# Kernel optimization log

Hardware: AMD Instinct MI355X
Metric: run time of the kernel (lower is better)

Reference implementation:

```python
import jax, jax.numpy as jnp
import numpy as np
import math

L, B, T, C, H, DH, V, MEM = 6, 2, 1024, 1024, 16, 64, 32000, 128

def _ln(x, g, b):
    m = jnp.mean(x, -1, keepdims=True)
    v = jnp.mean((x - m) ** 2, -1, keepdims=True)
    return (x - m) * jax.lax.rsqrt(v + 1e-5) * g + b

def _rel_shift(x):
    # x: [B,H,Q,K]; TransformerXL shift trick: pad zero col, reshape, drop first row
    b, h, q, k = x.shape
    xp = jnp.pad(x, ((0, 0), (0, 0), (0, 0), (1, 0)))
    xp = xp.reshape(b, h, k + 1, q)
    return xp[:, :, 1:, :].reshape(b, h, q, k)

def setup_inputs():
    key = jax.random.key(0)
    ks = jax.random.split(key, 12)
    d = {}
    d['idx'] = jax.random.randint(ks[0], (B, T), 0, V)
    d['mems'] = jax.random.normal(ks[1], (L, B, MEM, C), dtype=jnp.float32) * 0.02
    d['wte'] = jax.random.normal(ks[2], (V, C), dtype=jnp.float32) * 0.02
    d['ln1_g'] = jnp.ones((L, C), jnp.float32); d['ln1_b'] = jnp.zeros((L, C), jnp.float32)
    d['attn_w'] = jax.random.normal(ks[3], (L, C, 3 * C), dtype=jnp.float32) * 0.02
    d['attn_b'] = jnp.zeros((L, 3 * C), jnp.float32)
    d['proj_w'] = jax.random.normal(ks[4], (L, C, C), dtype=jnp.float32) * 0.02
    d['proj_b'] = jnp.zeros((L, C), jnp.float32)
    d['r_emb'] = jax.random.normal(ks[5], (L, H, DH), dtype=jnp.float32) * 0.02
    d['r_bias'] = jax.random.normal(ks[6], (L, H, DH), dtype=jnp.float32) * 0.02
    d['ln2_g'] = jnp.ones((L, C), jnp.float32); d['ln2_b'] = jnp.zeros((L, C), jnp.float32)
    d['fc_w'] = jax.random.normal(ks[7], (L, C, 4 * C), dtype=jnp.float32) * 0.02
    d['fc_b'] = jnp.zeros((L, 4 * C), jnp.float32)
    d['fc2_w'] = jax.random.normal(ks[8], (L, 4 * C, C), dtype=jnp.float32) * 0.02
    d['fc2_b'] = jnp.zeros((L, C), jnp.float32)
    d['lnf_g'] = jnp.ones((C,), jnp.float32); d['lnf_b'] = jnp.zeros((C,), jnp.float32)
    d['lm_w'] = jax.random.normal(ks[9], (C, V), dtype=jnp.float32) * 0.02
    return d

def _attn(x, mem, w, b, pw, pb, remb, rbias):
    Bx, Tx, Cx = x.shape
    cat = jnp.concatenate([mem, x], axis=1)          # [B,K,C], K = mem_len + Tx
    K = cat.shape[1]
    qkv = cat @ w + b
    q, k, v = jnp.split(qkv, 3, axis=-1)
    q = q.reshape(Bx, K, H, DH).transpose(0, 2, 1, 3)
    k = k.reshape(Bx, K, H, DH).transpose(0, 2, 1, 3)
    v = v.reshape(Bx, K, H, DH).transpose(0, 2, 1, 3)
    q = q + rbias[None, :, None, :]
    AC = jnp.einsum('bhid,bhjd->bhij', q, k)
    # BD: r is r_emb broadcast over positions, so q@r^T is constant over j
    s = jnp.einsum('bhid,hd->bhi', q, remb)
    BD = _rel_shift(jnp.broadcast_to(s[..., None], (Bx, H, K, K)))
    p = jax.nn.softmax((AC + BD) / math.sqrt(DH), axis=-1)
    y = jnp.einsum('bhij,bhjd->bhid', p, v).transpose(0, 2, 1, 3).reshape(Bx, K, Cx)
    y = y @ pw + pb
    new_mem = cat[:, -MEM:]
    return y, new_mem

def reference(idx, mems, wte, ln1_g, ln1_b, attn_w, attn_b, proj_w, proj_b, r_emb, r_bias, ln2_g, ln2_b, fc_w, fc_b, fc2_w, fc2_b, lnf_g, lnf_b, lm_w):
    x = wte[idx]                                      # [B,T,C]
    new_mems = []
    for l in range(L):
        h = _ln(x, ln1_g[l], ln1_b[l])
        y, nm = _attn(h, mems[l], attn_w[l], attn_b[l], proj_w[l], proj_b[l], r_emb[l], r_bias[l])
        h2 = _ln(y, ln2_g[l], ln2_b[l])
        m = jax.nn.gelu(h2 @ fc_w[l] + fc_b[l], approximate=False) @ fc2_w[l] + fc2_b[l]
        x = y + m                                     # note: residual onto attn output (length grows by MEM per layer)
        new_mems.append(nm)
    x = _ln(x, lnf_g, lnf_b)
    logits = x @ lm_w                                 # [B, L*MEM+T, V]
    return logits, jnp.stack(new_mems)
```

## Files before the change

kernel.cpp:

```cpp
#include <hip/hip_runtime.h>
#include <hip/hip_bf16.h>
#include <hip/hip_fp16.h>

#define LNUM 6
#define BB 2
#define TT 1024
#define CC 1024
#define HH 16
#define DHH 64
#define VV 32000
#define MM 128

typedef _Float16 f16;
typedef _Float16 f16x8 __attribute__((ext_vector_type(8)));
typedef float f32x4 __attribute__((ext_vector_type(4)));

__device__ __forceinline__ void g2lds16(const void* g, void* l) {
    __builtin_amdgcn_global_load_lds((const __attribute__((address_space(1))) void*)g,
                                     (__attribute__((address_space(3))) void*)l,
                                     16, 0, 0);
}

__device__ __forceinline__ float wred(float v) {
#pragma unroll
    for (int o = 32; o > 0; o >>= 1) v += __shfl_xor(v, o);
    return v;
}

__global__ __launch_bounds__(256)
void transpose_k(const float* __restrict__ W, f16* __restrict__ WT, int R, int Cc)
{
    __shared__ float tile[32][33];
    const size_t base = (size_t)blockIdx.z * R * Cc;
    const int c0 = blockIdx.x * 32, r0 = blockIdx.y * 32;
    const int tx = threadIdx.x & 31, ty = threadIdx.x >> 5;
#pragma unroll
    for (int i = 0; i < 32; i += 8)
        tile[ty + i][tx] = W[base + (size_t)(r0 + ty + i) * Cc + c0 + tx];
    __syncthreads();
#pragma unroll
    for (int i = 0; i < 32; i += 8)
        WT[base + (size_t)(c0 + ty + i) * R + r0 + tx] = (f16)tile[tx][ty + i];
}

__global__ __launch_bounds__(256)
void embed_k(const int* __restrict__ idx, const float* __restrict__ wte, float* __restrict__ X)
{
    const int row = blockIdx.x;
    const int id = idx[row];
    const float4* src = (const float4*)(wte + (size_t)id * CC);
    float4* dst = (float4*)(X + (size_t)row * CC);
    dst[threadIdx.x] = src[threadIdx.x];
}

__global__ __launch_bounds__(256)
void ln_k(const float* __restrict__ X, const float* __restrict__ g,
          const float* __restrict__ bta, f16* __restrict__ outH)
{
    const int row = blockIdx.x * 4 + (threadIdx.x >> 6);
    const int lane = threadIdx.x & 63;
    const float4* xr = (const float4*)(X + (size_t)row * CC);
    float4 v[4];
    float s = 0.f;
#pragma unroll
    for (int i = 0; i < 4; ++i) { v[i] = xr[i * 64 + lane]; s += v[i].x + v[i].y + v[i].z + v[i].w; }
    s = wred(s);
    const float mean = s * (1.f / CC);
    float q = 0.f;
#pragma unroll
    for (int i = 0; i < 4; ++i) {
        float a = v[i].x - mean, b = v[i].y - mean, c = v[i].z - mean, d = v[i].w - mean;
        q += a * a + b * b + c * c + d * d;
    }
    q = wred(q);
    const float rs = rsqrtf(q * (1.f / CC) + 1e-5f);
    const float4* g4 = (const float4*)g;
    const float4* b4 = (const float4*)bta;
    uint2* orow = (uint2*)(outH + (size_t)row * CC);
#pragma unroll
    for (int i = 0; i < 4; ++i) {
        float4 gg = g4[i * 64 + lane], bb = b4[i * 64 + lane];
        union { f16 h4[4]; uint2 u; } pk;
        pk.h4[0] = (f16)((v[i].x - mean) * rs * gg.x + bb.x);
        pk.h4[1] = (f16)((v[i].y - mean) * rs * gg.y + bb.y);
        pk.h4[2] = (f16)((v[i].z - mean) * rs * gg.z + bb.z);
        pk.h4[3] = (f16)((v[i].w - mean) * rs * gg.w + bb.w);
        orow[i * 64 + lane] = pk.u;
    }
}

__global__ __launch_bounds__(256)
void ln1cat_k(const float* __restrict__ X, const float* __restrict__ memsL,
              const float* __restrict__ g, const float* __restrict__ bta,
              f16* __restrict__ catH, float* __restrict__ nmOut,
              int K, int Kin)
{
    const int row = blockIdx.x * 4 + (threadIdx.x >> 6);
    const int lane = threadIdx.x & 63;
    const int b = row / K, rr = row % K;
    uint2* crow = (uint2*)(catH + (size_t)row * CC);
    if (rr < MM) {
        const float4* src = (const float4*)(memsL + ((size_t)b * MM + rr) * CC);
#pragma unroll
        for (int i = 0; i < 4; ++i) {
            float4 vv = src[i * 64 + lane];
            union { f16 h4[4]; uint2 u; } pk;
            pk.h4[0] = (f16)vv.x; pk.h4[1] = (f16)vv.y; pk.h4[2] = (f16)vv.z; pk.h4[3] = (f16)vv.w;
            crow[i * 64 + lane] = pk.u;
        }
        return;
    }
    const float4* xr = (const float4*)(X + ((size_t)b * Kin + (rr - MM)) * CC);
    float4 v[4];
    float s = 0.f;
#pragma unroll
    for (int i = 0; i < 4; ++i) { v[i] = xr[i * 64 + lane]; s += v[i].x + v[i].y + v[i].z + v[i].w; }
    s = wred(s);
    const float mean = s * (1.f / CC);
    float q = 0.f;
#pragma unroll
    for (int i = 0; i < 4; ++i) {
        float a = v[i].x - mean, b2 = v[i].y - mean, c = v[i].z - mean, d = v[i].w - mean;
        q += a * a + b2 * b2 + c * c + d * d;
    }
    q = wred(q);
    const float rs = rsqrtf(q * (1.f / CC) + 1e-5f);
    const float4* g4 = (const float4*)g;
    const float4* b4 = (const float4*)bta;
    float4* nm = nullptr;
    if (rr >= K - MM) nm = (float4*)(nmOut + ((size_t)b * MM + (rr - (K - MM))) * CC);
#pragma unroll
    for (int i = 0; i < 4; ++i) {
        float4 gg = g4[i * 64 + lane], bb = b4[i * 64 + lane];
        float4 o;
        o.x = (v[i].x - mean) * rs * gg.x + bb.x;
        o.y = (v[i].y - mean) * rs * gg.y + bb.y;
        o.z = (v[i].z - mean) * rs * gg.z + bb.z;
        o.w = (v[i].w - mean) * rs * gg.w + bb.w;
        union { f16 h4[4]; uint2 u; } pk;
        pk.h4[0] = (f16)o.x; pk.h4[1] = (f16)o.y; pk.h4[2] = (f16)o.z; pk.h4[3] = (f16)o.w;
        crow[i * 64 + lane] = pk.u;
        if (nm) nm[i * 64 + lane] = o;
    }
}

template <int EPI>
__global__ __launch_bounds__(256, 2)
void gemm_k(const f16* __restrict__ A, const f16* __restrict__ BT,
            const float* __restrict__ bias, const float* __restrict__ res,
            float* __restrict__ outF, f16* __restrict__ outH,
            int M, int N, int Kc)
{
    __shared__ f16 sA[128 * 32];
    __shared__ f16 sB[128 * 32];
    const int bn = blockIdx.x, bm = blockIdx.y;
    const int tid = threadIdx.x;
    const int w = tid >> 6, l = tid & 63;
    const int wr = w >> 1, wc = w & 1;
    const int lr = l & 15, lk = (l >> 4) * 8;

    f32x4 acc[4][4] = {};

    const int ar = w * 32 + (l >> 2);
    const int ak = (l & 3) * 8;
    const f16* gA = A + (size_t)(bm * 128 + ar) * Kc + ak;
    const f16* gB = BT + (size_t)(bn * 128 + ar) * Kc + ak;
    f16* lA = sA + w * 1024;
    f16* lB = sB + w * 1024;

    for (int kt = 0; kt < Kc; kt += 32) {
        g2lds16(gA + kt, lA);
        g2lds16(gA + kt + (size_t)16 * Kc, lA + 512);
        g2lds16(gB + kt, lB);
        g2lds16(gB + kt + (size_t)16 * Kc, lB + 512);
        __syncthreads();
        f16x8 af[4], bf[4];
#pragma unroll
        for (int mi = 0; mi < 4; ++mi) af[mi] = *(const f16x8*)&sA[(wr * 64 + mi * 16 + lr) * 32 + lk];
#pragma unroll
        for (int ni = 0; ni < 4; ++ni) bf[ni] = *(const f16x8*)&sB[(wc * 64 + ni * 16 + lr) * 32 + lk];
#pragma unroll
        for (int mi = 0; mi < 4; ++mi)
#pragma unroll
            for (int ni = 0; ni < 4; ++ni)
                acc[mi][ni] = __builtin_amdgcn_mfma_f32_16x16x32_f16(af[mi], bf[ni], acc[mi][ni], 0, 0, 0);
        __syncthreads();
    }

    const int orow0 = bm * 128 + wr * 64 + (l >> 4) * 4;
    const int ocol0 = bn * 128 + wc * 64 + lr;
#pragma unroll
    for (int mi = 0; mi < 4; ++mi)
#pragma unroll
        for (int ni = 0; ni < 4; ++ni) {
            const int col = ocol0 + ni * 16;
            const float bv = (EPI >= 1) ? bias[col] : 0.f;
#pragma unroll
            for (int r = 0; r < 4; ++r) {
                const int row = orow0 + mi * 16 + r;
                float v = acc[mi][ni][r] + bv;
                if (EPI == 2) {
                    v = 0.5f * v * (1.f + erff(v * 0.70710678118654752f));
                    outH[(size_t)row * N + col] = (f16)v;
                } else if (EPI == 4) {
                    outH[(size_t)row * N + col] = (f16)v;
                } else if (EPI == 3) {
                    v += res[(size_t)row * N + col];
                    outF[(size_t)row * N + col] = v;
                } else {
                    outF[(size_t)row * N + col] = v;
                }
            }
        }
}

template <int EPI>
__global__ __launch_bounds__(512, 2)
void gemm256_k(const f16* __restrict__ A, const f16* __restrict__ BT,
               const float* __restrict__ bias,
               float* __restrict__ outF, f16* __restrict__ outH,
               int M, int N, int Kc)
{
    __shared__ char ldsbuf[131072];
    char* ldsA = ldsbuf;
    char* ldsB = ldsbuf + 65536;

    const int nbn = N >> 8;
    const int nwg = gridDim.x;
    {
    }
    int id = blockIdx.x;
    const int qq = nwg >> 3, rr8 = nwg & 7;
    const int xcd = id & 7, pos = id >> 3;
    const int wgid = (xcd < rr8 ? xcd * (qq + 1) : rr8 * (qq + 1) + (xcd - rr8) * qq) + pos;
    const int bm = wgid / nbn, bn = wgid % nbn;

    const int t_ = threadIdx.x;
    const int w = t_ >> 6, l = t_ & 63;
    const int wm = w >> 2, wn = w & 3;
    const int lr = l & 15, lhi = l >> 4;

    const f16* gA = A + (size_t)bm * 256 * Kc;
    const f16* gB = BT + (size_t)bn * 256 * Kc;

    auto stage = [&](const f16* Gbase, char* ldsHalf, int kt) {
#pragma unroll
        for (int ii = 0; ii < 2; ++ii) {
            const int gb = (w << 1) + ii;
            const int s = (gb << 6) + l;
            const int row = s >> 3, grp = s & 7;
            g2lds16(Gbase + (size_t)row * Kc + kt + ((grp ^ (row & 7)) << 3),
                    ldsHalf + gb * 1024);
        }
    };
    auto rdfrag = [&](const char* halfBase, int rowInHalf, int ks) -> f16x8 {
        return *(const f16x8*)(halfBase + rowInHalf * 128 +
                               ((((ks << 2) + lhi) ^ (rowInHalf & 7)) << 4));
    };

    f32x4 acc[8][4] = {};
    f16x8 aA[4][2], blo[2][2], bhi[2][2];

    const int NT = Kc >> 6;
    const char* aHalf0 = ldsA + wm * 16384;
    const char* aHalf1 = ldsA + 32768 + wm * 16384;
    const char* bHalf0 = ldsB + (wn >> 1) * 16384;
    const char* bHalf1 = ldsB + 32768 + (wn >> 1) * 16384;
    const int brow = (wn & 1) * 64;

    stage(gA, ldsA + 0, 0);
    stage(gA + (size_t)128 * Kc, ldsA + 16384, 0);
    stage(gB, ldsB + 0, 0);
    stage(gB + (size_t)128 * Kc, ldsB + 16384, 0);
    stage(gB, ldsB + 32768, 64);
    stage(gB + (size_t)128 * Kc, ldsB + 49152, 64);
    asm volatile("s_waitcnt vmcnt(0)" ::: "memory");
    __builtin_amdgcn_s_barrier();

#define MFMA_QUAD(MQ, NQ, BR)                                                            \
    __builtin_amdgcn_s_setprio(1);                                                       \
    _Pragma("unroll") for (int mf = 0; mf < 4; ++mf)                                     \
    _Pragma("unroll") for (int nf = 0; nf < 2; ++nf)                                     \
    _Pragma("unroll") for (int ks = 0; ks < 2; ++ks)                                     \
        acc[(MQ)*4 + mf][(NQ)*2 + nf] =                                                  \
            __builtin_amdgcn_mfma_f32_16x16x32_f16(aA[mf][ks], BR[nf][ks],               \
                                                   acc[(MQ)*4 + mf][(NQ)*2 + nf], 0, 0, 0); \
    __builtin_amdgcn_s_setprio(0);

#define PHASE_SYNC()                                          \
    __builtin_amdgcn_s_barrier();                             \
    asm volatile("s_waitcnt lgkmcnt(0)" ::: "memory");        \
    __builtin_amdgcn_sched_barrier(0);

    for (int t = 0; t < NT; t += 2) {
        const bool pf0 = (t + 2) < NT;
        const int kb = (t + 1) << 6, kc2 = (t + 2) << 6, kd = (t + 3) << 6;

#pragma unroll
        for (int mf = 0; mf < 4; ++mf)
#pragma unroll
            for (int ks = 0; ks < 2; ++ks) aA[mf][ks] = rdfrag(aHalf0, mf * 16 + lr, ks);
#pragma unroll
        for (int nf = 0; nf < 2; ++nf)
#pragma unroll
            for (int ks = 0; ks < 2; ++ks) blo[nf][ks] = rdfrag(bHalf0, brow + nf * 16 + lr, ks);
        stage(gA, ldsA + 32768, kb);
        PHASE_SYNC();
        MFMA_QUAD(0, 0, blo);
        __builtin_amdgcn_s_barrier();

#pragma unroll
        for (int nf = 0; nf < 2; ++nf)
#pragma unroll
            for (int ks = 0; ks < 2; ++ks) bhi[nf][ks] = rdfrag(bHalf0, brow + 32 + nf * 16 + lr, ks);
        stage(gA + (size_t)128 * Kc, ldsA + 49152, kb);
        PHASE_SYNC();
        MFMA_QUAD(0, 1, bhi);
        __builtin_amdgcn_s_barrier();

#pragma unroll
        for (int mf = 0; mf < 4; ++mf)
#pragma unroll
            for (int ks = 0; ks < 2; ++ks) aA[mf][ks] = rdfrag(aHalf0, 64 + mf * 16 + lr, ks);
        if (pf0) stage(gB, ldsB + 0, kc2);
        PHASE_SYNC();
        MFMA_QUAD(1, 0, blo);
        __builtin_amdgcn_s_barrier();

        if (pf0) {
            stage(gB + (size_t)128 * Kc, ldsB + 16384, kc2);
            asm volatile("s_waitcnt vmcnt(4)" ::: "memory");
        } else {
            asm volatile("s_waitcnt vmcnt(0)" ::: "memory");
        }
        PHASE_SYNC();
        MFMA_QUAD(1, 1, bhi);
        __builtin_amdgcn_s_barrier();

#pragma unroll
        for (int mf = 0; mf < 4; ++mf)
#pragma unroll
            for (int ks = 0; ks < 2; ++ks) aA[mf][ks] = rdfrag(aHalf1, mf * 16 + lr, ks);
#pragma unroll
        for (int nf = 0; nf < 2; ++nf)
#pragma unroll
            for (int ks = 0; ks < 2; ++ks) blo[nf][ks] = rdfrag(bHalf1, brow + nf * 16 + lr, ks);
        if (pf0) stage(gA, ldsA + 0, kc2);
        PHASE_SYNC();
        MFMA_QUAD(0, 0, blo);
        __builtin_amdgcn_s_barrier();

#pragma unroll
        for (int nf = 0; nf < 2; ++nf)
#pragma unroll
            for (int ks = 0; ks < 2; ++ks) bhi[nf][ks] = rdfrag(bHalf1, brow + 32 + nf * 16 + lr, ks);
        if (pf0) stage(gA + (size_t)128 * Kc, ldsA + 16384, kc2);
        PHASE_SYNC();
        MFMA_QUAD(0, 1, bhi);
        __builtin_amdgcn_s_barrier();

#pragma unroll
        for (int mf = 0; mf < 4; ++mf)
#pragma unroll
            for (int ks = 0; ks < 2; ++ks) aA[mf][ks] = rdfrag(aHalf1, 64 + mf * 16 + lr, ks);
        if (pf0) stage(gB, ldsB + 32768, kd);
        PHASE_SYNC();
        MFMA_QUAD(1, 0, blo);
        __builtin_amdgcn_s_barrier();

        if (pf0) {
            stage(gB + (size_t)128 * Kc, ldsB + 49152, kd);
            asm volatile("s_waitcnt vmcnt(4)" ::: "memory");
        } else {
            asm volatile("s_waitcnt vmcnt(0)" ::: "memory");
        }
        PHASE_SYNC();
        MFMA_QUAD(1, 1, bhi);
        __builtin_amdgcn_s_barrier();
    }
#undef MFMA_QUAD
#undef PHASE_SYNC

    const int rb0 = bm * 256 + wm * 128 + lhi * 4;
    const int cb0 = bn * 256 + wn * 64 + lr;
#pragma unroll
    for (int mf = 0; mf < 8; ++mf)
#pragma unroll
        for (int nf = 0; nf < 4; ++nf) {
            const int col = cb0 + nf * 16;
            const float bv = (EPI >= 1) ? bias[col] : 0.f;
#pragma unroll
            for (int r = 0; r < 4; ++r) {
                const int row = rb0 + mf * 16 + r;
                float v = acc[mf][nf][r] + bv;
                if (EPI == 2) {
                    v = 0.5f * v * (1.f + erff(v * 0.70710678118654752f));
                    outH[(size_t)row * N + col] = (f16)v;
                } else if (EPI == 4) {
                    outH[(size_t)row * N + col] = (f16)v;
                } else {
                    outF[(size_t)row * N + col] = v;
                }
            }
        }
}

__global__ __launch_bounds__(256)
void attn_k(const f16* __restrict__ qkv, const float* __restrict__ remb,
            const float* __restrict__ rbias, f16* __restrict__ yH, int K)
{
    __shared__ f16 K_lds[64 * 64];
    __shared__ f16 Vt_lds[64 * 64];
    __shared__ f16 P_lds[64 * 64];
    __shared__ float s_s[66];

    const int b = blockIdx.x >> 4, h = blockIdx.x & 15;
    const int i0 = blockIdx.y * 64;
    const int t = threadIdx.x;
    const int w = t >> 6, l = t & 63;
    const int c = l & 15, g = l >> 4;

    const f16* qg = qkv + (size_t)b * K * 3072 + h * 64;
    const f16* kg = qg + 1024;
    const f16* vg = qg + 2048;
    const float* rb = rbias + h * 64;
    const float* re = remb + h * 64;

    f16x8 qf[2];
    {
        const int qrow = i0 + w * 16 + c;
#pragma unroll
        for (int ks = 0; ks < 2; ++ks) {
            f16x8 raw = *(const f16x8*)(qg + (size_t)qrow * 3072 + ks * 32 + g * 8);
            f16x8 o;
#pragma unroll
            for (int j = 0; j < 8; ++j) o[j] = (f16)((float)raw[j] + rb[ks * 32 + g * 8 + j]);
            qf[ks] = o;
        }
    }
    if (t < 65) {
        float sv = 0.f;
        const int i = i0 + t;
        if (i < K) {
            const f16* qr = qg + (size_t)i * 3072;
#pragma unroll
            for (int d8 = 0; d8 < 8; ++d8) {
                f16x8 v8 = *(const f16x8*)(qr + d8 * 8);
#pragma unroll
                for (int j = 0; j < 8; ++j) sv += ((float)v8[j] + rb[d8 * 8 + j]) * re[d8 * 8 + j];
            }
        }
        s_s[t] = sv;
    }
    __syncthreads();

    float sA[4], sB[4];
#pragma unroll
    for (int r = 0; r < 4; ++r) {
        sA[r] = s_s[w * 16 + g * 4 + r];
        sB[r] = s_s[w * 16 + g * 4 + r + 1];
    }

    float m_run[4] = {-1e30f, -1e30f, -1e30f, -1e30f};
    float l_run[4] = {0.f, 0.f, 0.f, 0.f};
    f32x4 yacc[4] = {};

    const int kb = t >> 4, db = t & 15;

    for (int j0 = 0; j0 < K; j0 += 64) {
#pragma unroll
        for (int i = 0; i < 2; ++i) {
            const int slot = w * 128 + i * 64 + l;
            const int row = slot >> 3, grp = slot & 7;
            const f16* src = kg + (size_t)(j0 + row) * 3072 + ((grp ^ (row & 7)) * 8);
            g2lds16(src, (char*)K_lds + (size_t)(w * 128 + i * 64) * 16);
        }
        {
            union { uint2 u; f16 hh[4]; } rowv[4];
#pragma unroll
            for (int i = 0; i < 4; ++i)
                rowv[i].u = *(const uint2*)(vg + (size_t)(j0 + kb * 4 + i) * 3072 + db * 4);
#pragma unroll
            for (int j = 0; j < 4; ++j) {
                union { uint2 u; f16 hh[4]; } colv;
#pragma unroll
                for (int i = 0; i < 4; ++i) colv.hh[i] = rowv[i].hh[j];
                const int d = db * 4 + j;
                *(uint2*)((char*)Vt_lds + d * 128 + ((kb * 8) ^ ((d & 7) << 4))) = colv.u;
            }
        }
        __syncthreads();

        f32x4 sc[4] = {};
#pragma unroll
        for (int tt = 0; tt < 4; ++tt) {
            const int row = tt * 16 + c;
#pragma unroll
            for (int ks = 0; ks < 2; ++ks) {
                f16x8 kf = *(const f16x8*)((char*)K_lds + row * 128 + ((ks * 64 + g * 16) ^ ((row & 7) << 4)));
                sc[tt] = __builtin_amdgcn_mfma_f32_16x16x32_f16(qf[ks], kf, sc[tt], 0, 0, 0);
            }
        }

        float p[4][4];
#pragma unroll
        for (int tt = 0; tt < 4; ++tt)
#pragma unroll
            for (int r = 0; r < 4; ++r) {
                const int gi = i0 + w * 16 + g * 4 + r;
                const int gj = j0 + tt * 16 + c;
                const float bd = (gj <= gi) ? sA[r] : ((gj == gi + 1) ? 0.f : sB[r]);
                p[tt][r] = (sc[tt][r] + bd) * 0.125f;
            }
#pragma unroll
        for (int r = 0; r < 4; ++r) {
            float mx = fmaxf(fmaxf(p[0][r], p[1][r]), fmaxf(p[2][r], p[3][r]));
            mx = fmaxf(mx, __shfl_xor(mx, 1));
            mx = fmaxf(mx, __shfl_xor(mx, 2));
            mx = fmaxf(mx, __shfl_xor(mx, 4));
            mx = fmaxf(mx, __shfl_xor(mx, 8));
            const float mnew = fmaxf(m_run[r], mx);
            const float f = __expf(m_run[r] - mnew);
            m_run[r] = mnew;
            float ss = 0.f;
#pragma unroll
            for (int tt = 0; tt < 4; ++tt) {
                const float e = __expf(p[tt][r] - mnew);
                p[tt][r] = e;
                ss += e;
            }
            ss += __shfl_xor(ss, 1);
            ss += __shfl_xor(ss, 2);
            ss += __shfl_xor(ss, 4);
            ss += __shfl_xor(ss, 8);
            l_run[r] = l_run[r] * f + ss;
#pragma unroll
            for (int tt = 0; tt < 4; ++tt) yacc[tt][r] *= f;
        }

#pragma unroll
        for (int tt = 0; tt < 4; ++tt)
#pragma unroll
            for (int r = 0; r < 4; ++r) {
                const int q = w * 16 + g * 4 + r;
                *(f16*)((char*)P_lds + q * 128 + (((tt * 16 + c) * 2) ^ ((q & 7) << 4))) = (f16)p[tt][r];
            }
        asm volatile("s_waitcnt lgkmcnt(0)" ::: "memory");
        __builtin_amdgcn_sched_barrier(0);

        {
            const int qrow = w * 16 + c;
            f16x8 pa[2];
#pragma unroll
            for (int ks = 0; ks < 2; ++ks)
                pa[ks] = *(const f16x8*)((char*)P_lds + qrow * 128 + ((ks * 64 + g * 16) ^ ((qrow & 7) << 4)));
#pragma unroll
            for (int tt = 0; tt < 4; ++tt) {
                const int drow = tt * 16 + c;
#pragma unroll
                for (int ks = 0; ks < 2; ++ks) {
                    f16x8 vb = *(const f16x8*)((char*)Vt_lds + drow * 128 + ((ks * 64 + g * 16) ^ ((drow & 7) << 4)));
                    yacc[tt] = __builtin_amdgcn_mfma_f32_16x16x32_f16(pa[ks], vb, yacc[tt], 0, 0, 0);
                }
            }
        }
        __syncthreads();
    }

#pragma unroll
    for (int r = 0; r < 4; ++r) {
        const float inv = 1.f / l_run[r];
        const int row = i0 + w * 16 + g * 4 + r;
        f16* dst = yH + (size_t)(b * K + row) * CC + h * 64;
#pragma unroll
        for (int tt = 0; tt < 4; ++tt)
            dst[tt * 16 + c] = (f16)(yacc[tt][r] * inv);
    }
}

extern "C" void kernel_launch(void* const* d_in, const int* in_sizes, int n_in,
                              void* d_out, int out_size, void* d_ws, size_t ws_size,
                              hipStream_t stream)
{
    (void)in_sizes; (void)n_in; (void)out_size; (void)ws_size;
    const int*   idx    = (const int*)  d_in[0];
    const float* mems   = (const float*)d_in[1];
    const float* wte    = (const float*)d_in[2];
    const float* ln1_g  = (const float*)d_in[3];
    const float* ln1_b  = (const float*)d_in[4];
    const float* attn_w = (const float*)d_in[5];
    const float* attn_b = (const float*)d_in[6];
    const float* proj_w = (const float*)d_in[7];
    const float* proj_b = (const float*)d_in[8];
    const float* r_emb  = (const float*)d_in[9];
    const float* r_bias = (const float*)d_in[10];
    const float* ln2_g  = (const float*)d_in[11];
    const float* ln2_b  = (const float*)d_in[12];
    const float* fc_w   = (const float*)d_in[13];
    const float* fc_b   = (const float*)d_in[14];
    const float* fc2_w  = (const float*)d_in[15];
    const float* fc2_b  = (const float*)d_in[16];
    const float* lnf_g  = (const float*)d_in[17];
    const float* lnf_b  = (const float*)d_in[18];
    const float* lm_w   = (const float*)d_in[19];
    float* out = (float*)d_out;

    char* wp = (char*)d_ws; size_t off = 0;
    auto carve = [&](size_t bytes) -> void* {
        void* p = wp + off; off += (bytes + 255) & ~(size_t)255; return p;
    };
    const int KMAX = TT + LNUM * MM;
    f16*  attn_wT = (f16*) carve((size_t)LNUM * 3 * CC * CC * 2);
    f16*  proj_wT = (f16*) carve((size_t)LNUM * CC * CC * 2);
    f16*  fc_wT   = (f16*) carve((size_t)LNUM * 4 * CC * CC * 2);
    f16*  fc2_wT  = (f16*) carve((size_t)LNUM * 4 * CC * CC * 2);
    f16*  lm_wT   = (f16*) carve((size_t)VV * CC * 2);
    float* x0     = (float*)carve((size_t)BB * KMAX * CC * 4);
    float* x1     = (float*)carve((size_t)BB * KMAX * CC * 4);
    f16*  catH    = (f16*) carve((size_t)BB * KMAX * CC * 2);
    f16*  qkv16   = (f16*) carve((size_t)BB * KMAX * 3 * CC * 2);
    f16*  yH      = (f16*) carve((size_t)BB * KMAX * CC * 2);
    float* yp     = (float*)carve((size_t)BB * KMAX * CC * 4);
    f16*  h2H     = (f16*) carve((size_t)BB * KMAX * CC * 2);
    f16*  a1H     = (f16*) carve((size_t)BB * KMAX * 4 * CC * 2);
    f16*  xfH     = (f16*) carve((size_t)BB * KMAX * CC * 2);

    transpose_k<<<dim3(3 * CC / 32, CC / 32, LNUM), 256, 0, stream>>>(attn_w, attn_wT, CC, 3 * CC);
    transpose_k<<<dim3(CC / 32, CC / 32, LNUM),     256, 0, stream>>>(proj_w, proj_wT, CC, CC);
    transpose_k<<<dim3(4 * CC / 32, CC / 32, LNUM), 256, 0, stream>>>(fc_w, fc_wT, CC, 4 * CC);
    transpose_k<<<dim3(CC / 32, 4 * CC / 32, LNUM), 256, 0, stream>>>(fc2_w, fc2_wT, 4 * CC, CC);
    transpose_k<<<dim3(VV / 32, CC / 32, 1),        256, 0, stream>>>(lm_w, lm_wT, CC, VV);

    embed_k<<<BB * TT, 256, 0, stream>>>(idx, wte, x0);

    const size_t LOGITS = (size_t)BB * KMAX * VV;
    float* xcur = x0; float* xnxt = x1;
    for (int l = 0; l < LNUM; ++l) {
        const int Kin = TT + MM * l;
        const int K = Kin + MM;
        const int Mrows = BB * K;
        const int nbm = Mrows / 256;
        ln1cat_k<<<Mrows / 4, 256, 0, stream>>>(xcur, mems + (size_t)l * BB * MM * CC,
                                                ln1_g + l * CC, ln1_b + l * CC,
                                                catH, out + LOGITS + (size_t)l * BB * MM * CC, K, Kin);
        gemm256_k<4><<<nbm * (3 * CC / 256), 512, 0, stream>>>(
            catH, attn_wT + (size_t)l * 3 * CC * CC, attn_b + (size_t)l * 3 * CC,
            nullptr, qkv16, Mrows, 3 * CC, CC);
        attn_k<<<dim3(BB * HH, K / 64), 256, 0, stream>>>(
            qkv16, r_emb + (size_t)l * HH * DHH, r_bias + (size_t)l * HH * DHH, yH, K);
        gemm_k<1><<<dim3(CC / 128, Mrows / 128), 256, 0, stream>>>(
            yH, proj_wT + (size_t)l * CC * CC, proj_b + (size_t)l * CC, nullptr,
            yp, nullptr, Mrows, CC, CC);
        ln_k<<<Mrows / 4, 256, 0, stream>>>(yp, ln2_g + l * CC, ln2_b + l * CC, h2H);
        gemm256_k<2><<<nbm * (4 * CC / 256), 512, 0, stream>>>(
            h2H, fc_wT + (size_t)l * 4 * CC * CC, fc_b + (size_t)l * 4 * CC,
            nullptr, a1H, Mrows, 4 * CC, CC);
        gemm_k<3><<<dim3(CC / 128, Mrows / 128), 256, 0, stream>>>(
            a1H, fc2_wT + (size_t)l * 4 * CC * CC, fc2_b + (size_t)l * CC, yp,
            xnxt, nullptr, Mrows, CC, 4 * CC);
        float* tmp = xcur; xcur = xnxt; xnxt = tmp;
    }
    ln_k<<<(BB * KMAX) / 4, 256, 0, stream>>>(xcur, lnf_g, lnf_b, xfH);
    gemm256_k<0><<<(BB * KMAX / 256) * (VV / 256), 512, 0, stream>>>(
        xfH, lm_wT, nullptr, out, nullptr, BB * KMAX, VV, CC);
}
```

Baseline: 2.350 ms.

## Use lazy softmax rescaling, column-major 256 GEMM tiles, and 128-tile QKV/FC GEMMs

Flash attention now rescales the running max only when some lane's block max exceeds the current max by more than 8. It also defers the row-sum cross-lane reduction to the epilogue, which removes shuffles and exp/rescale work from the inner loop. The 256-tile GEMM now walks tiles with the M index fastest, so workgroups that share a weight column tile run close together. The QKV and FC1 projections move from the 256-tile kernel to the 128-tile gemm_k, trading per-block reuse for more blocks. The running max starts at 0 rather than -inf, so precision depends on scores staying bounded.

```diff
diff --git a/kernel.cpp b/kernel.cpp
--- a/kernel.cpp
+++ b/kernel.cpp
@@ -225,15 +225,13 @@
     char* ldsA = ldsbuf;
     char* ldsB = ldsbuf + 65536;
 
-    const int nbn = N >> 8;
+    const int nbm = M >> 8;
     const int nwg = gridDim.x;
-    {
-    }
     int id = blockIdx.x;
     const int qq = nwg >> 3, rr8 = nwg & 7;
     const int xcd = id & 7, pos = id >> 3;
     const int wgid = (xcd < rr8 ? xcd * (qq + 1) : rr8 * (qq + 1) + (xcd - rr8) * qq) + pos;
-    const int bm = wgid / nbn, bn = wgid % nbn;
+    const int bm = wgid % nbm, bn = wgid / nbm;
 
     const int t_ = threadIdx.x;
     const int w = t_ >> 6, l = t_ & 63;
@@ -461,8 +459,8 @@
         sB[r] = s_s[w * 16 + g * 4 + r + 1];
     }
 
-    float m_run[4] = {-1e30f, -1e30f, -1e30f, -1e30f};
-    float l_run[4] = {0.f, 0.f, 0.f, 0.f};
+    float m_run[4] = {0.f, 0.f, 0.f, 0.f};
+    float psum[4] = {0.f, 0.f, 0.f, 0.f};
     f32x4 yacc[4] = {};
 
     const int kb = t >> 4, db = t & 15;
@@ -512,30 +510,41 @@
                 const float bd = (gj <= gi) ? sA[r] : ((gj == gi + 1) ? 0.f : sB[r]);
                 p[tt][r] = (sc[tt][r] + bd) * 0.125f;
             }
+
+        float lmax[4];
+        bool need = false;
 #pragma unroll
         for (int r = 0; r < 4; ++r) {
-            float mx = fmaxf(fmaxf(p[0][r], p[1][r]), fmaxf(p[2][r], p[3][r]));
-            mx = fmaxf(mx, __shfl_xor(mx, 1));
-            mx = fmaxf(mx, __shfl_xor(mx, 2));
-            mx = fmaxf(mx, __shfl_xor(mx, 4));
-            mx = fmaxf(mx, __shfl_xor(mx, 8));
-            const float mnew = fmaxf(m_run[r], mx);
-            const float f = __expf(m_run[r] - mnew);
-            m_run[r] = mnew;
+            lmax[r] = fmaxf(fmaxf(p[0][r], p[1][r]), fmaxf(p[2][r], p[3][r]));
+            need |= (lmax[r] > m_run[r] + 8.f);
+        }
+        if (__any(need)) {
+#pragma unroll
+            for (int r = 0; r < 4; ++r) {
+                float mx = lmax[r];
+                mx = fmaxf(mx, __shfl_xor(mx, 1));
+                mx = fmaxf(mx, __shfl_xor(mx, 2));
+                mx = fmaxf(mx, __shfl_xor(mx, 4));
+                mx = fmaxf(mx, __shfl_xor(mx, 8));
+                if (mx > m_run[r]) {
+                    const float f = __expf(m_run[r] - mx);
+                    m_run[r] = mx;
+                    psum[r] *= f;
+#pragma unroll
+                    for (int tt = 0; tt < 4; ++tt) yacc[tt][r] *= f;
+                }
+            }
+        }
+#pragma unroll
+        for (int r = 0; r < 4; ++r) {
             float ss = 0.f;
 #pragma unroll
             for (int tt = 0; tt < 4; ++tt) {
-                const float e = __expf(p[tt][r] - mnew);
+                const float e = __expf(p[tt][r] - m_run[r]);
                 p[tt][r] = e;
                 ss += e;
             }
-            ss += __shfl_xor(ss, 1);
-            ss += __shfl_xor(ss, 2);
-            ss += __shfl_xor(ss, 4);
-            ss += __shfl_xor(ss, 8);
-            l_run[r] = l_run[r] * f + ss;
-#pragma unroll
-            for (int tt = 0; tt < 4; ++tt) yacc[tt][r] *= f;
+            psum[r] += ss;
         }
 
 #pragma unroll
@@ -569,7 +578,12 @@
 
 #pragma unroll
     for (int r = 0; r < 4; ++r) {
-        const float inv = 1.f / l_run[r];
+        float ps = psum[r];
+        ps += __shfl_xor(ps, 1);
+        ps += __shfl_xor(ps, 2);
+        ps += __shfl_xor(ps, 4);
+        ps += __shfl_xor(ps, 8);
+        const float inv = 1.f / ps;
         const int row = i0 + w * 16 + g * 4 + r;
         f16* dst = yH + (size_t)(b * K + row) * CC + h * 64;
 #pragma unroll
@@ -639,12 +653,11 @@
         const int Kin = TT + MM * l;
         const int K = Kin + MM;
         const int Mrows = BB * K;
-        const int nbm = Mrows / 256;
         ln1cat_k<<<Mrows / 4, 256, 0, stream>>>(xcur, mems + (size_t)l * BB * MM * CC,
                                                 ln1_g + l * CC, ln1_b + l * CC,
                                                 catH, out + LOGITS + (size_t)l * BB * MM * CC, K, Kin);
-        gemm256_k<4><<<nbm * (3 * CC / 256), 512, 0, stream>>>(
-            catH, attn_wT + (size_t)l * 3 * CC * CC, attn_b + (size_t)l * 3 * CC,
+        gemm_k<4><<<dim3(3 * CC / 128, Mrows / 128), 256, 0, stream>>>(
+            catH, attn_wT + (size_t)l * 3 * CC * CC, attn_b + (size_t)l * 3 * CC, nullptr,
             nullptr, qkv16, Mrows, 3 * CC, CC);
         attn_k<<<dim3(BB * HH, K / 64), 256, 0, stream>>>(
             qkv16, r_emb + (size_t)l * HH * DHH, r_bias + (size_t)l * HH * DHH, yH, K);
@@ -652,8 +665,8 @@
             yH, proj_wT + (size_t)l * CC * CC, proj_b + (size_t)l * CC, nullptr,
             yp, nullptr, Mrows, CC, CC);
         ln_k<<<Mrows / 4, 256, 0, stream>>>(yp, ln2_g + l * CC, ln2_b + l * CC, h2H);
-        gemm256_k<2><<<nbm * (4 * CC / 256), 512, 0, stream>>>(
-            h2H, fc_wT + (size_t)l * 4 * CC * CC, fc_b + (size_t)l * 4 * CC,
+        gemm_k<2><<<dim3(4 * CC / 128, Mrows / 128), 256, 0, stream>>>(
+            h2H, fc_wT + (size_t)l * 4 * CC * CC, fc_b + (size_t)l * 4 * CC, nullptr,
             nullptr, a1H, Mrows, 4 * CC, CC);
         gemm_k<3><<<dim3(CC / 128, Mrows / 128), 256, 0, stream>>>(
             a1H, fc2_wT + (size_t)l * 4 * CC * CC, fc2_b + (size_t)l * CC, yp,
```

After: 2.163 ms. -7.9%, faster.
